# Performance work log

Measured on AMD Instinct MI355X. Metric: run time of the kernel, lower is better.

Reference implementation:

```python
import jax, jax.numpy as jnp
import numpy as np

I, H, O = 3, 50, 1

def setup_inputs() -> dict:
    key = jax.random.key(0)
    ks = jax.random.split(key, 7)
    B, T = 4096, 512
    s_ih = 1.0 / np.sqrt(H)
    x = jax.random.normal(ks[0], (B, T, I), dtype=jnp.float32)
    W_ih = jax.random.uniform(ks[1], (3 * H, I), jnp.float32, -s_ih, s_ih)
    W_hh = jax.random.uniform(ks[2], (3 * H, H), jnp.float32, -s_ih, s_ih)
    b_ih = jax.random.uniform(ks[3], (3 * H,), jnp.float32, -s_ih, s_ih)
    b_hh = jax.random.uniform(ks[4], (3 * H,), jnp.float32, -s_ih, s_ih)
    W_fc = jax.random.uniform(ks[5], (O, H), jnp.float32, -s_ih, s_ih)
    b_fc = jax.random.uniform(ks[6], (O,), jnp.float32, -s_ih, s_ih)
    return {"x": x, "W_ih": W_ih, "W_hh": W_hh, "b_ih": b_ih, "b_hh": b_hh,
            "W_fc": W_fc, "b_fc": b_fc}

def _gru_last_hidden(x, W_ih, W_hh, b_ih, b_hh):
    # x: [B, T, I]. Precompute input projections for all timesteps (one big GEMM).
    B, T, _ = x.shape
    gi = jnp.einsum('bti,gi->btg', x, W_ih) + b_ih  # [B, T, 3H]
    gi = jnp.moveaxis(gi, 1, 0)  # [T, B, 3H] for scan over time

    W_hr, W_hz, W_hn = W_hh[:H], W_hh[H:2*H], W_hh[2*H:]
    b_hr, b_hz, b_hn = b_hh[:H], b_hh[H:2*H], b_hh[2*H:]

    def step(h, gi_t):
        gir, giz, gin = gi_t[:, :H], gi_t[:, H:2*H], gi_t[:, 2*H:]
        r = jax.nn.sigmoid(gir + h @ W_hr.T + b_hr)
        z = jax.nn.sigmoid(giz + h @ W_hz.T + b_hz)
        n = jnp.tanh(gin + r * (h @ W_hn.T + b_hn))
        h_new = (1.0 - z) * n + z * h
        return h_new, None

    h0 = jnp.zeros((B, H), dtype=x.dtype)
    h_last, _ = jax.lax.scan(step, h0, gi)
    return h_last  # [B, H]

def reference(x, W_ih, W_hh, b_ih, b_hh, W_fc, b_fc):
    h_last = _gru_last_hidden(x, W_ih, W_hh, b_ih, b_hh)
    out = h_last @ W_fc.T + b_fc  # [B, 1]
    return out.squeeze(-1)  # [B]
```

## Files before the change

### kernel.cpp

```cpp
#include <hip/hip_runtime.h>
#include <hip/hip_bf16.h>

#define T_LEN 512
#define HID 50
#define NBATCH 4096

using short8  = __attribute__((ext_vector_type(8))) short;
using floatx4 = __attribute__((ext_vector_type(4))) float;

__device__ __forceinline__ float sigm(float v) {
  return __builtin_amdgcn_rcpf(1.0f + __builtin_amdgcn_exp2f(-1.442695041f * v));
}
__device__ __forceinline__ float tanh_f(float v) {
  return 1.0f - 2.0f * __builtin_amdgcn_rcpf(1.0f + __builtin_amdgcn_exp2f(2.885390082f * v));
}

__global__ __launch_bounds__(256, 1)
void gru_mfma_kernel(const float* __restrict__ x,
                     const float* __restrict__ W_ih,
                     const float* __restrict__ W_hh,
                     const float* __restrict__ b_ih,
                     const float* __restrict__ b_hh,
                     const float* __restrict__ W_fc,
                     const float* __restrict__ b_fc,
                     float* __restrict__ out) {
  __shared__ alignas(16) unsigned char lds[16384];
  char* xs   = (char*)lds;
  char* hbuf = (char*)lds + 12288;

  const int tid  = threadIdx.x;
  const int lane = tid & 63;
  const int w    = tid >> 6;
  const int ucol = lane & 15;
  const int kg   = (lane >> 4) & 3;
  const int b0   = blockIdx.x * 16;
  const int u    = 16 * w + ucol;
  const bool uv  = (u < HID);

  float c_r[4], c_z[4], c_ni[4], c_nh[4], wfc[4];
  float ur[4][3], uz[4][3], un[4][3];
#pragma unroll
  for (int r = 0; r < 4; ++r) {
    const int uu = 16 * w + 4 * kg + r;
    const bool vr = (uu < HID);
    c_r[r]  = vr ? (b_ih[uu] + b_hh[uu]) : 0.f;
    c_z[r]  = vr ? (b_ih[50 + uu] + b_hh[50 + uu]) : 0.f;
    c_ni[r] = vr ? b_ih[100 + uu] : 0.f;
    c_nh[r] = vr ? b_hh[100 + uu] : 0.f;
    wfc[r]  = vr ? W_fc[uu] : 0.f;
#pragma unroll
    for (int c = 0; c < 3; ++c) {
      ur[r][c] = vr ? W_ih[uu * 3 + c] : 0.f;
      uz[r][c] = vr ? W_ih[(50 + uu) * 3 + c] : 0.f;
      un[r][c] = vr ? W_ih[(100 + uu) * 3 + c] : 0.f;
    }
  }

  short8 Wf[3][2];
#pragma unroll
  for (int g = 0; g < 3; ++g) {
    const int row = uv ? (g * 50 + u) : 0;
    const float* Wrow = W_hh + row * HID;
#pragma unroll
    for (int f = 0; f < 2; ++f) {
      union { short a[8]; short8 s; } ph;
#pragma unroll
      for (int e = 0; e < 8; ++e) {
        const int k = 32 * f + 8 * kg + e;
        const float v = (uv && k < HID) ? Wrow[k] : 0.f;
        __hip_bfloat16 bh = __float2bfloat16(v);
        ph.a[e] = *(short*)&bh;
      }
      Wf[g][f] = ph.s;
    }
  }

  ((float4*)hbuf)[tid] = make_float4(0.f, 0.f, 0.f, 0.f);

  float h[4] = {0.f, 0.f, 0.f, 0.f};

  const int hrow = ucol * 128;
  const int axr  = (ucol & 7) << 4;
  const int soff = hrow + ((32 * w + 8 * kg) ^ axr);
  const floatx4 z4 = {0.f, 0.f, 0.f, 0.f};

  for (int tc = 0; tc < 8; ++tc) {
    {
      const int sm = tid >> 4, seg = tid & 15;
      const float* xb = x + (size_t)(b0 + sm) * (T_LEN * 3) + tc * 192 + seg * 12;
      const float4 v0 = *(const float4*)(xb + 0);
      const float4 v1 = *(const float4*)(xb + 4);
      const float4 v2 = *(const float4*)(xb + 8);
      const float vv[12] = {v0.x, v0.y, v0.z, v0.w, v1.x, v1.y, v1.z, v1.w, v2.x, v2.y, v2.z, v2.w};
#pragma unroll
      for (int jj = 0; jj < 12; ++jj) {
        const int i = seg * 12 + jj;
        *(float*)(xs + (i / 3) * 192 + (i % 3) * 64 + sm * 4) = vv[jj];
      }
    }
    __syncthreads();

#pragma unroll 2
    for (int s = 0; s < 64; ++s) {
      const int par = s & 1;
      const char* rp = hbuf + par * 2048;
      char*       wp = hbuf + (par ^ 1) * 2048;

      const float x0 = *(const float*)(xs + s * 192 +   0 + ucol * 4);
      const float x1 = *(const float*)(xs + s * 192 +  64 + ucol * 4);
      const float x2 = *(const float*)(xs + s * 192 + 128 + ucol * 4);

      const short8 H0 = *(const short8*)(rp + hrow + ((16 * kg)      ^ axr));
      const short8 H1 = *(const short8*)(rp + hrow + ((16 * kg + 64) ^ axr));

      floatx4 aR = __builtin_amdgcn_mfma_f32_16x16x32_bf16(Wf[0][0], H0, z4, 0, 0, 0);
      aR = __builtin_amdgcn_mfma_f32_16x16x32_bf16(Wf[0][1], H1, aR, 0, 0, 0);
      floatx4 aZ = __builtin_amdgcn_mfma_f32_16x16x32_bf16(Wf[1][0], H0, z4, 0, 0, 0);
      aZ = __builtin_amdgcn_mfma_f32_16x16x32_bf16(Wf[1][1], H1, aZ, 0, 0, 0);
      floatx4 aN = __builtin_amdgcn_mfma_f32_16x16x32_bf16(Wf[2][0], H0, z4, 0, 0, 0);
      aN = __builtin_amdgcn_mfma_f32_16x16x32_bf16(Wf[2][1], H1, aN, 0, 0, 0);

      unsigned int hw[2];
#pragma unroll
      for (int q = 0; q < 2; ++q) {
        unsigned int pk = 0;
#pragma unroll
        for (int j = 0; j < 2; ++j) {
          const int r = 2 * q + j;
          const float gr = fmaf(x0, ur[r][0], fmaf(x1, ur[r][1], fmaf(x2, ur[r][2], c_r[r])));
          const float gz = fmaf(x0, uz[r][0], fmaf(x1, uz[r][1], fmaf(x2, uz[r][2], c_z[r])));
          const float gn = fmaf(x0, un[r][0], fmaf(x1, un[r][1], fmaf(x2, un[r][2], c_ni[r])));
          const float rr = sigm(aR[r] + gr);
          const float zz = sigm(aZ[r] + gz);
          const float omz = 1.0f - zz;
          const float zh  = zz * h[r];
          const float nn  = tanh_f(gn + rr * (aN[r] + c_nh[r]));
          h[r] = fmaf(nn, omz, zh);
          __hip_bfloat16 bh = __float2bfloat16(h[r]);
          pk |= (unsigned int)(*(const unsigned short*)&bh) << (16 * j);
        }
        hw[q] = pk;
      }
      *(unsigned long long*)(wp + soff) =
          (unsigned long long)hw[0] | ((unsigned long long)hw[1] << 32);
      __syncthreads();
    }
  }

  float p = h[0] * wfc[0] + h[1] * wfc[1] + h[2] * wfc[2] + h[3] * wfc[3];
  p += __shfl_xor(p, 16);
  p += __shfl_xor(p, 32);
  if (lane < 16) {
    *(float*)(lds + (w * 16 + ucol) * 4) = p;
  }
  __syncthreads();
  if (tid < 16) {
    float ssum = 0.f;
#pragma unroll
    for (int ww = 0; ww < 4; ++ww) ssum += *(const float*)(lds + (ww * 16 + tid) * 4);
    out[b0 + tid] = ssum + b_fc[0];
  }
}

extern "C" void kernel_launch(void* const* d_in, const int* in_sizes, int n_in,
                              void* d_out, int out_size, void* d_ws, size_t ws_size,
                              hipStream_t stream) {
  const float* x    = (const float*)d_in[0];
  const float* W_ih = (const float*)d_in[1];
  const float* W_hh = (const float*)d_in[2];
  const float* b_ih = (const float*)d_in[3];
  const float* b_hh = (const float*)d_in[4];
  const float* W_fc = (const float*)d_in[5];
  const float* b_fc = (const float*)d_in[6];
  float* out = (float*)d_out;

  dim3 grid(NBATCH / 16);
  dim3 block(256);
  gru_mfma_kernel<<<grid, block, 0, stream>>>(x, W_ih, W_hh, b_ih, b_hh, W_fc, b_fc, out);
}
```

Baseline: 216.6 us.

## Fold input projection and biases into the recurrent MFMA via augmented K columns

Packs x (as split hi/lo bf16 pairs), a constant one and the bias terms into the unused K padding slots (50-60) of the hidden-state tile. The input projection and biases are then computed inside the existing MFMAs, plus one extra MFMA for the n-gate input part. This removes the per-step scalar FMAs and the per-thread W_ih/bias registers. In exchange, wave 3 has to pack x into the shared buffer at every step, and the x-loading offset shifts by one timestep to prefetch the next x.

```diff
diff --git a/kernel.cpp b/kernel.cpp
--- a/kernel.cpp
+++ b/kernel.cpp
@@ -13,6 +13,13 @@
 }
 __device__ __forceinline__ float tanh_f(float v) {
   return 1.0f - 2.0f * __builtin_amdgcn_rcpf(1.0f + __builtin_amdgcn_exp2f(2.885390082f * v));
+}
+__device__ __forceinline__ unsigned short bf16hi(float v) {
+  __hip_bfloat16 b = __float2bfloat16(v);
+  return *(unsigned short*)&b;
+}
+__device__ __forceinline__ float bf16tof(unsigned short u) {
+  return __uint_as_float((unsigned int)u << 16);
 }
 
 __global__ __launch_bounds__(256, 1)
@@ -37,48 +44,91 @@
   const int u    = 16 * w + ucol;
   const bool uv  = (u < HID);
 
-  float c_r[4], c_z[4], c_ni[4], c_nh[4], wfc[4];
-  float ur[4][3], uz[4][3], un[4][3];
+  float wfc[4];
 #pragma unroll
   for (int r = 0; r < 4; ++r) {
     const int uu = 16 * w + 4 * kg + r;
-    const bool vr = (uu < HID);
-    c_r[r]  = vr ? (b_ih[uu] + b_hh[uu]) : 0.f;
-    c_z[r]  = vr ? (b_ih[50 + uu] + b_hh[50 + uu]) : 0.f;
-    c_ni[r] = vr ? b_ih[100 + uu] : 0.f;
-    c_nh[r] = vr ? b_hh[100 + uu] : 0.f;
-    wfc[r]  = vr ? W_fc[uu] : 0.f;
-#pragma unroll
-    for (int c = 0; c < 3; ++c) {
-      ur[r][c] = vr ? W_ih[uu * 3 + c] : 0.f;
-      uz[r][c] = vr ? W_ih[(50 + uu) * 3 + c] : 0.f;
-      un[r][c] = vr ? W_ih[(100 + uu) * 3 + c] : 0.f;
-    }
+    wfc[r] = (uu < HID) ? W_fc[uu] : 0.f;
   }
 
   short8 Wf[3][2];
+  short8 WfC;
 #pragma unroll
   for (int g = 0; g < 3; ++g) {
-    const int row = uv ? (g * 50 + u) : 0;
-    const float* Wrow = W_hh + row * HID;
 #pragma unroll
     for (int f = 0; f < 2; ++f) {
       union { short a[8]; short8 s; } ph;
 #pragma unroll
       for (int e = 0; e < 8; ++e) {
         const int k = 32 * f + 8 * kg + e;
-        const float v = (uv && k < HID) ? Wrow[k] : 0.f;
-        __hip_bfloat16 bh = __float2bfloat16(v);
-        ph.a[e] = *(short*)&bh;
+        float v = 0.f; bool lo = false;
+        if (uv) {
+          if (g < 2) {
+            if (k < HID)        v = W_hh[(g * 50 + u) * HID + k];
+            else if (k <= 52)   v = W_ih[(g * 50 + u) * 3 + (k - 50)];
+            else if (k == 53)   v = b_ih[g * 50 + u] + b_hh[g * 50 + u];
+            else if (k <= 56)   v = W_ih[(g * 50 + u) * 3 + (k - 54)];
+            else if (k <= 59) { v = W_ih[(g * 50 + u) * 3 + (k - 57)]; lo = true; }
+            else if (k == 60) { v = b_ih[g * 50 + u] + b_hh[g * 50 + u]; lo = true; }
+          } else {
+            if (k < HID)        v = W_hh[(100 + u) * HID + k];
+            else if (k == 53)   v = b_hh[100 + u];
+            else if (k == 60) { v = b_hh[100 + u]; lo = true; }
+          }
+        }
+        unsigned short el;
+        if (lo) { const unsigned short hi = bf16hi(v); el = bf16hi(v - bf16tof(hi)); }
+        else    { el = bf16hi(v); }
+        ph.a[e] = (short)el;
       }
       Wf[g][f] = ph.s;
     }
   }
+  {
+    union { short a[8]; short8 s; } ph;
+#pragma unroll
+    for (int e = 0; e < 8; ++e) {
+      const int k = 32 + 8 * kg + e;
+      float v = 0.f; bool lo = false;
+      if (uv) {
+        if (k >= 50 && k <= 52)      v = W_ih[(100 + u) * 3 + (k - 50)];
+        else if (k == 53)            v = b_ih[100 + u];
+        else if (k >= 54 && k <= 56) v = W_ih[(100 + u) * 3 + (k - 54)];
+        else if (k >= 57 && k <= 59) { v = W_ih[(100 + u) * 3 + (k - 57)]; lo = true; }
+        else if (k == 60)            { v = b_ih[100 + u]; lo = true; }
+      }
+      unsigned short el;
+      if (lo) { const unsigned short hi = bf16hi(v); el = bf16hi(v - bf16tof(hi)); }
+      else    { el = bf16hi(v); }
+      ph.a[e] = (short)el;
+    }
+    WfC = ph.s;
+  }
 
   ((float4*)hbuf)[tid] = make_float4(0.f, 0.f, 0.f, 0.f);
+  __syncthreads();
+  if (tid < 16) {
+    const int m = tid;
+    char* p0 = hbuf + m * 128;
+    const int xr = (m & 7) << 4;
+    unsigned short hi[3], lo[3];
+#pragma unroll
+    for (int c = 0; c < 3; ++c) {
+      const float xv = x[(size_t)(b0 + m) * (T_LEN * 3) + c];
+      hi[c] = bf16hi(xv);
+      lo[c] = bf16hi(xv - bf16tof(hi[c]));
+    }
+#pragma unroll
+    for (int c = 0; c < 3; ++c) {
+      *(unsigned short*)(p0 + ((2 * (50 + c)) ^ xr)) = hi[c];
+      *(unsigned short*)(p0 + ((2 * (54 + c)) ^ xr)) = lo[c];
+      *(unsigned short*)(p0 + ((2 * (57 + c)) ^ xr)) = hi[c];
+    }
+    *(unsigned short*)(p0 + ((2 * 53) ^ xr)) = 0x3F80;
+    *(unsigned short*)(p0 + ((2 * 60) ^ xr)) = 0x3F80;
+  }
 
   float h[4] = {0.f, 0.f, 0.f, 0.f};
-
   const int hrow = ucol * 128;
   const int axr  = (ucol & 7) << 4;
   const int soff = hrow + ((32 * w + 8 * kg) ^ axr);
@@ -87,11 +137,19 @@
   for (int tc = 0; tc < 8; ++tc) {
     {
       const int sm = tid >> 4, seg = tid & 15;
-      const float* xb = x + (size_t)(b0 + sm) * (T_LEN * 3) + tc * 192 + seg * 12;
-      const float4 v0 = *(const float4*)(xb + 0);
-      const float4 v1 = *(const float4*)(xb + 4);
-      const float4 v2 = *(const float4*)(xb + 8);
-      const float vv[12] = {v0.x, v0.y, v0.z, v0.w, v1.x, v1.y, v1.z, v1.w, v2.x, v2.y, v2.z, v2.w};
+      const float* xb = x + (size_t)(b0 + sm) * (T_LEN * 3) + tc * 192 + 3 + seg * 12;
+      float vv[12];
+      if (tc == 7 && seg == 15) {
+#pragma unroll
+        for (int j = 0; j < 12; ++j) vv[j] = (j < 9) ? xb[j] : 0.f;
+      } else {
+        const float4 v0 = *(const float4*)(xb + 0);
+        const float4 v1 = *(const float4*)(xb + 4);
+        const float4 v2 = *(const float4*)(xb + 8);
+        vv[0]=v0.x; vv[1]=v0.y; vv[2]=v0.z; vv[3]=v0.w;
+        vv[4]=v1.x; vv[5]=v1.y; vv[6]=v1.z; vv[7]=v1.w;
+        vv[8]=v2.x; vv[9]=v2.y; vv[10]=v2.z; vv[11]=v2.w;
+      }
 #pragma unroll
       for (int jj = 0; jj < 12; ++jj) {
         const int i = seg * 12 + jj;
@@ -105,10 +163,6 @@
       const int par = s & 1;
       const char* rp = hbuf + par * 2048;
       char*       wp = hbuf + (par ^ 1) * 2048;
-
-      const float x0 = *(const float*)(xs + s * 192 +   0 + ucol * 4);
-      const float x1 = *(const float*)(xs + s * 192 +  64 + ucol * 4);
-      const float x2 = *(const float*)(xs + s * 192 + 128 + ucol * 4);
 
       const short8 H0 = *(const short8*)(rp + hrow + ((16 * kg)      ^ axr));
       const short8 H1 = *(const short8*)(rp + hrow + ((16 * kg + 64) ^ axr));
@@ -119,30 +173,43 @@
       aZ = __builtin_amdgcn_mfma_f32_16x16x32_bf16(Wf[1][1], H1, aZ, 0, 0, 0);
       floatx4 aN = __builtin_amdgcn_mfma_f32_16x16x32_bf16(Wf[2][0], H0, z4, 0, 0, 0);
       aN = __builtin_amdgcn_mfma_f32_16x16x32_bf16(Wf[2][1], H1, aN, 0, 0, 0);
-
-      unsigned int hw[2];
-#pragma unroll
-      for (int q = 0; q < 2; ++q) {
-        unsigned int pk = 0;
-#pragma unroll
-        for (int j = 0; j < 2; ++j) {
-          const int r = 2 * q + j;
-          const float gr = fmaf(x0, ur[r][0], fmaf(x1, ur[r][1], fmaf(x2, ur[r][2], c_r[r])));
-          const float gz = fmaf(x0, uz[r][0], fmaf(x1, uz[r][1], fmaf(x2, uz[r][2], c_z[r])));
-          const float gn = fmaf(x0, un[r][0], fmaf(x1, un[r][1], fmaf(x2, un[r][2], c_ni[r])));
-          const float rr = sigm(aR[r] + gr);
-          const float zz = sigm(aZ[r] + gz);
-          const float omz = 1.0f - zz;
-          const float zh  = zz * h[r];
-          const float nn  = tanh_f(gn + rr * (aN[r] + c_nh[r]));
-          h[r] = fmaf(nn, omz, zh);
-          __hip_bfloat16 bh = __float2bfloat16(h[r]);
-          pk |= (unsigned int)(*(const unsigned short*)&bh) << (16 * j);
-        }
-        hw[q] = pk;
-      }
-      *(unsigned long long*)(wp + soff) =
-          (unsigned long long)hw[0] | ((unsigned long long)hw[1] << 32);
+      const floatx4 aC = __builtin_amdgcn_mfma_f32_16x16x32_bf16(WfC, H1, z4, 0, 0, 0);
+
+      unsigned short hs[4];
+#pragma unroll
+      for (int r = 0; r < 4; ++r) {
+        const float rr  = sigm(aR[r]);
+        const float zz  = sigm(aZ[r]);
+        const float omz = 1.0f - zz;
+        const float zh  = zz * h[r];
+        const float nn  = tanh_f(fmaf(rr, aN[r], aC[r]));
+        h[r] = fmaf(nn, omz, zh);
+        hs[r] = bf16hi(h[r]);
+      }
+
+      if (w < 3) {
+        const unsigned long long pk =
+            (unsigned long long)hs[0] | ((unsigned long long)hs[1] << 16) |
+            ((unsigned long long)hs[2] << 32) | ((unsigned long long)hs[3] << 48);
+        *(unsigned long long*)(wp + soff) = pk;
+      } else {
+        const float x0 = *(const float*)(xs + s * 192 +   0 + ucol * 4);
+        const float x1 = *(const float*)(xs + s * 192 +  64 + ucol * 4);
+        const float x2 = *(const float*)(xs + s * 192 + 128 + ucol * 4);
+        const unsigned short h0 = bf16hi(x0), h1 = bf16hi(x1), h2 = bf16hi(x2);
+        const unsigned short l0 = bf16hi(x0 - bf16tof(h0));
+        const unsigned short l1 = bf16hi(x1 - bf16tof(h1));
+        const unsigned short l2 = bf16hi(x2 - bf16tof(h2));
+        const unsigned short ONE = 0x3F80;
+        const unsigned short v0 = (kg == 0) ? hs[0] : (kg == 1) ? h2 : (kg == 2) ? l2 : ONE;
+        const unsigned short v1 = (kg == 0) ? hs[1] : (kg == 1) ? ONE : (kg == 2) ? h0 : (unsigned short)0;
+        const unsigned short v2 = (kg == 0) ? h0    : (kg == 1) ? l0  : (kg == 2) ? h1 : (unsigned short)0;
+        const unsigned short v3 = (kg == 0) ? h1    : (kg == 1) ? l1  : (kg == 2) ? h2 : (unsigned short)0;
+        const unsigned long long pk =
+            (unsigned long long)v0 | ((unsigned long long)v1 << 16) |
+            ((unsigned long long)v2 << 32) | ((unsigned long long)v3 << 48);
+        *(unsigned long long*)(wp + soff) = pk;
+      }
       __syncthreads();
     }
   }
```

Result: slower. 226.5 us (+4.6%).
